# Kernel optimization log

Measured on AMD Instinct MI355X. Metric: run time of the kernel, lower is better.

The kernel has to match this reference:

```python
import jax, jax.numpy as jnp
import numpy as np

N_NODES = 100000
N_EDGES = 1600000
N_FEAT = 64
HIDDEN = 64
N_GRAPHS = 256


def setup_inputs() -> dict:
    key = jax.random.key(0)
    ks = jax.random.split(key, 8)
    x = jax.random.normal(ks[0], (N_NODES, N_FEAT), dtype=jnp.float32)
    edge_index = jax.random.randint(ks[1], (2, N_EDGES), 0, N_NODES, dtype=jnp.int64)
    batch = jnp.sort(jax.random.randint(ks[2], (N_NODES,), 0, N_GRAPHS, dtype=jnp.int64))
    W1 = jax.random.normal(ks[3], (N_FEAT, HIDDEN), dtype=jnp.float32) / np.sqrt(N_FEAT)
    b1 = jnp.zeros((HIDDEN,), dtype=jnp.float32)
    W2 = jax.random.normal(ks[4], (HIDDEN, HIDDEN), dtype=jnp.float32) / np.sqrt(HIDDEN)
    b2 = jnp.zeros((HIDDEN,), dtype=jnp.float32)
    Wfc = jax.random.normal(ks[5], (HIDDEN, 1), dtype=jnp.float32) / np.sqrt(HIDDEN)
    bfc = jnp.zeros((1,), dtype=jnp.float32)
    return {"x": x, "edge_index": edge_index, "batch": batch,
            "W1": W1, "b1": b1, "W2": W2, "b2": b2, "Wfc": Wfc, "bfc": bfc}


def _gcn_conv(x, W, b, src, dst, norm, n_nodes):
    # h = X W, then symmetric-normalized scatter-add aggregation at dst
    h = x @ W  # [N, H]
    msg = h[src] * norm[:, None]  # [E+N, H] gather + scale
    agg = jax.ops.segment_sum(msg, dst, num_segments=n_nodes)
    return agg + b


def reference(x, edge_index, batch, W1, b1, W2, b2, Wfc, bfc):
    n = x.shape[0]
    loops = jnp.arange(n, dtype=edge_index.dtype)
    src = jnp.concatenate([edge_index[0], loops])  # add self-loops (GCNConv default)
    dst = jnp.concatenate([edge_index[1], loops])
    deg = jax.ops.segment_sum(jnp.ones_like(dst, dtype=x.dtype), dst, num_segments=n)
    dinv = jnp.where(deg > 0, jax.lax.rsqrt(deg), 0.0)
    norm = dinv[src] * dinv[dst]  # D^-1/2 (A+I) D^-1/2

    h = jax.nn.relu(_gcn_conv(x, W1, b1, src, dst, norm, n))  # dropout = identity (eval)
    h = jax.nn.relu(_gcn_conv(h, W2, b2, src, dst, norm, n))

    # global mean pool over graphs
    sums = jax.ops.segment_sum(h, batch, num_segments=N_GRAPHS)
    counts = jax.ops.segment_sum(jnp.ones((n,), dtype=h.dtype), batch, num_segments=N_GRAPHS)
    pooled = sums / jnp.maximum(counts, 1.0)[:, None]  # [G, H]
    return jax.nn.sigmoid(pooled @ Wfc + bfc)  # [G, 1]
```

## Files before the change

kernel.cpp:

```cpp
#include <hip/hip_runtime.h>
#include <hip/hip_fp16.h>
#include <math.h>

#define N_NODES  100000
#define N_EDGES  1600000
#define NF       64
#define N_GRAPHS 256

#define BSH   7
#define NB    ((N_NODES + 127) / 128)
#define BCAP  2600

typedef float f32x2 __attribute__((ext_vector_type(2)));

__global__ void k_zerocur(int* __restrict__ bucketCur) {
    int i = blockIdx.x * blockDim.x + threadIdx.x;
    if (i < NB) bucketCur[i] = 0;
}

__global__ __launch_bounds__(1024) void k_bscatter(const int* __restrict__ src,
                                                   const int* __restrict__ dst,
                                                   int* __restrict__ bucketCur,
                                                   int* __restrict__ scratch) {
    __shared__ int hist[NB];
    __shared__ int bbase[NB];
    int t = threadIdx.x;
    for (int i = t; i < NB; i += 1024) hist[i] = 0;
    __syncthreads();
    int e0 = (blockIdx.x * 1024 + t) * 8;
    int d[8], s[8], r[8];
    bool act = (e0 + 7) < N_EDGES;
    if (act) {
        *(int4*)&d[0] = *(const int4*)(dst + e0);
        *(int4*)&d[4] = *(const int4*)(dst + e0 + 4);
        *(int4*)&s[0] = *(const int4*)(src + e0);
        *(int4*)&s[4] = *(const int4*)(src + e0 + 4);
#pragma unroll
        for (int k = 0; k < 8; ++k) r[k] = atomicAdd(&hist[d[k] >> BSH], 1);
    }
    __syncthreads();
    for (int i = t; i < NB; i += 1024)
        if (hist[i]) bbase[i] = atomicAdd(&bucketCur[i], hist[i]);
    __syncthreads();
    if (act) {
#pragma unroll
        for (int k = 0; k < 8; ++k) {
            int b = d[k] >> BSH;
            int pos = bbase[b] + r[k];
            if (pos < BCAP)
                scratch[b * BCAP + pos] = ((d[k] & 127) << 17) | s[k];
        }
    }
}

__global__ __launch_bounds__(1024) void k_bscan(const int* __restrict__ bucketCur,
                                                int* __restrict__ bucketPtr,
                                                int* __restrict__ rowptr) {
    int t = threadIdx.x;
    __shared__ int ps[1024];
    int v = (t < NB) ? min(bucketCur[t], BCAP) : 0;
    ps[t] = v;
    __syncthreads();
#pragma unroll
    for (int off = 1; off < 1024; off <<= 1) {
        int u = (t >= off) ? ps[t - off] : 0;
        __syncthreads();
        ps[t] += u;
        __syncthreads();
    }
    if (t < NB) bucketPtr[t] = ps[t] - v;
    if (t == NB - 1) {
        bucketPtr[NB] = ps[t];
        rowptr[N_NODES] = ps[t];
    }
}

__global__ __launch_bounds__(256) void k_bfinal(const int* __restrict__ bucketCur,
                                                const int* __restrict__ bucketPtr,
                                                const int* __restrict__ scratch,
                                                int* __restrict__ rowptr,
                                                float* __restrict__ dinv,
                                                int* __restrict__ col) {
    int b = blockIdx.x;
    int cnt  = min(bucketCur[b], BCAP);
    int base = bucketPtr[b];
    int node0 = b << BSH;
    __shared__ int hist[128];
    __shared__ int escan[128];
    __shared__ int ps[128];
    __shared__ int rnk[BCAP];
    int t = threadIdx.x;
    if (t < 128) hist[t] = 0;
    __syncthreads();
    const int* sp = scratch + b * BCAP;
    for (int j = t; j < cnt; j += 256)
        rnk[j] = atomicAdd(&hist[sp[j] >> 17], 1);
    __syncthreads();
    int hv = (t < 128) ? hist[t] : 0;
    if (t < 128) ps[t] = hv;
    __syncthreads();
#pragma unroll
    for (int off = 1; off < 128; off <<= 1) {
        int u = 0;
        if (t < 128 && t >= off) u = ps[t - off];
        __syncthreads();
        if (t < 128) ps[t] += u;
        __syncthreads();
    }
    if (t < 128) {
        int excl = ps[t] - hv;
        escan[t] = excl;
        int node = node0 + t;
        if (node < N_NODES) {
            rowptr[node] = base + excl;
            dinv[node] = rsqrtf((float)(hv + 1));
        }
    }
    __syncthreads();
    for (int j = t; j < cnt; j += 256) {
        int pk = sp[j];
        col[base + escan[pk >> 17] + rnk[j]] = pk & 0x1FFFF;
    }
}

__global__ __launch_bounds__(256) void k_gemm(const float* __restrict__ X,
                                              const float* __restrict__ W,
                                              const float* __restrict__ bias,
                                              const float* __restrict__ dinv,
                                              int* __restrict__ Ah8) {
    __shared__ float Ws[64][64];
    __shared__ float Xs[64][68];
    int t  = threadIdx.x;
    int n0 = blockIdx.x * 64;

    for (int i = t; i < 64 * 64; i += 256) Ws[i >> 6][i & 63] = W[i];

#pragma unroll
    for (int p = 0; p < 4; ++p) {
        int flat = p * 256 + t;
        int nl = flat >> 4;
        int kg = flat & 15;
        int node = n0 + nl;
        float4 v = make_float4(0.f, 0.f, 0.f, 0.f);
        if (node < N_NODES) {
            v = *(const float4*)(X + (size_t)node * NF + kg * 4);
            if (bias) {
                v.x += bias[kg * 4 + 0]; v.x = v.x > 0.f ? v.x : 0.f;
                v.y += bias[kg * 4 + 1]; v.y = v.y > 0.f ? v.y : 0.f;
                v.z += bias[kg * 4 + 2]; v.z = v.z > 0.f ? v.z : 0.f;
                v.w += bias[kg * 4 + 3]; v.w = v.w > 0.f ? v.w : 0.f;
            }
        }
        Xs[kg * 4 + 0][nl] = v.x;
        Xs[kg * 4 + 1][nl] = v.y;
        Xs[kg * 4 + 2][nl] = v.z;
        Xs[kg * 4 + 3][nl] = v.w;
    }
    __syncthreads();

    int tx = t & 15;
    int ty = t >> 4;
    float acc[4][4];
#pragma unroll
    for (int i = 0; i < 4; ++i)
#pragma unroll
        for (int j = 0; j < 4; ++j) acc[i][j] = 0.f;

#pragma unroll 8
    for (int k = 0; k < 64; ++k) {
        float4 wv = *(const float4*)&Ws[k][tx * 4];
        float4 xv = *(const float4*)&Xs[k][ty * 4];
        acc[0][0] += xv.x * wv.x; acc[0][1] += xv.x * wv.y;
        acc[0][2] += xv.x * wv.z; acc[0][3] += xv.x * wv.w;
        acc[1][0] += xv.y * wv.x; acc[1][1] += xv.y * wv.y;
        acc[1][2] += xv.y * wv.z; acc[1][3] += xv.y * wv.w;
        acc[2][0] += xv.z * wv.x; acc[2][1] += xv.z * wv.y;
        acc[2][2] += xv.z * wv.z; acc[2][3] += xv.z * wv.w;
        acc[3][0] += xv.w * wv.x; acc[3][1] += xv.w * wv.y;
        acc[3][2] += xv.w * wv.z; acc[3][3] += xv.w * wv.w;
    }

#pragma unroll
    for (int i = 0; i < 4; ++i) {
        int node = n0 + ty * 4 + i;
        if (node < N_NODES) {
            float dv = dinv[node];
            int pk = 0;
            pk = __builtin_amdgcn_cvt_pk_fp8_f32(acc[i][0] * dv, acc[i][1] * dv, pk, false);
            pk = __builtin_amdgcn_cvt_pk_fp8_f32(acc[i][2] * dv, acc[i][3] * dv, pk, true);
            Ah8[(size_t)node * 16 + tx] = pk;
        }
    }
}

__global__ __launch_bounds__(256) void k_pull(const int* __restrict__ rowptr,
                                              const int* __restrict__ col,
                                              const float* __restrict__ dinv,
                                              const int* __restrict__ Ah8,
                                              float* __restrict__ B) {
    int n    = (blockIdx.x * blockDim.x + threadIdx.x) >> 6;
    int lane = threadIdx.x & 63;
    if (n >= N_NODES) return;
    int slot = lane >> 3;
    int oct  = lane & 7;
    int beg = rowptr[n];
    int cnt = rowptr[n + 1] - beg + 1;

    float acc0 = 0.f, acc1 = 0.f, acc2 = 0.f, acc3 = 0.f;
    float acc4 = 0.f, acc5 = 0.f, acc6 = 0.f, acc7 = 0.f;

    for (int base = slot; base < cnt; base += 32) {
        int cidx[4];
#pragma unroll
        for (int p = 0; p < 4; ++p) {
            int idx = base + p * 8;
            cidx[p] = (idx < cnt) ? ((idx == 0) ? n : col[beg + idx - 1]) : -1;
        }
#pragma unroll
        for (int p = 0; p < 4; ++p) {
            int s = cidx[p];
            if (s >= 0) {
                int2 raw = *(const int2*)(Ah8 + (size_t)s * 16 + oct * 2);
                f32x2 f0 = __builtin_amdgcn_cvt_pk_f32_fp8(raw.x, false);
                f32x2 f1 = __builtin_amdgcn_cvt_pk_f32_fp8(raw.x, true);
                f32x2 f2 = __builtin_amdgcn_cvt_pk_f32_fp8(raw.y, false);
                f32x2 f3 = __builtin_amdgcn_cvt_pk_f32_fp8(raw.y, true);
                acc0 += f0.x; acc1 += f0.y;
                acc2 += f1.x; acc3 += f1.y;
                acc4 += f2.x; acc5 += f2.y;
                acc6 += f3.x; acc7 += f3.y;
            }
        }
    }
#pragma unroll
    for (int off = 8; off < 64; off <<= 1) {
        acc0 += __shfl_down(acc0, off);
        acc1 += __shfl_down(acc1, off);
        acc2 += __shfl_down(acc2, off);
        acc3 += __shfl_down(acc3, off);
        acc4 += __shfl_down(acc4, off);
        acc5 += __shfl_down(acc5, off);
        acc6 += __shfl_down(acc6, off);
        acc7 += __shfl_down(acc7, off);
    }
    if (slot == 0) {
        float dv = dinv[n];
        float4 o0 = make_float4(acc0 * dv, acc1 * dv, acc2 * dv, acc3 * dv);
        float4 o1 = make_float4(acc4 * dv, acc5 * dv, acc6 * dv, acc7 * dv);
        *(float4*)(B + (size_t)n * NF + oct * 8)     = o0;
        *(float4*)(B + (size_t)n * NF + oct * 8 + 4) = o1;
    }
}

__device__ __forceinline__ int lower_bound_i(const int* __restrict__ a, int n, int key) {
    int lo = 0, hi = n;
    while (lo < hi) {
        int mid = (lo + hi) >> 1;
        if (a[mid] < key) lo = mid + 1; else hi = mid;
    }
    return lo;
}

__global__ __launch_bounds__(512) void k_pool_final(const float* __restrict__ B,
                                                    const int* __restrict__ batch,
                                                    const float* __restrict__ b2,
                                                    const float* __restrict__ Wfc,
                                                    const float* __restrict__ bfc,
                                                    float* __restrict__ out) {
    int g = blockIdx.x;
    __shared__ int s_lo, s_hi;
    int t = threadIdx.x;
    if (t == 0) {
        s_lo = lower_bound_i(batch, N_NODES, g);
        s_hi = lower_bound_i(batch, N_NODES, g + 1);
    }
    __syncthreads();
    int lo = s_lo, hi = s_hi;
    int ln = t >> 6, lane = t & 63;
    float bias = b2[lane];
    float acc = 0.0f;
    for (int n = lo + ln; n < hi; n += 8) {
        float v = B[(size_t)n * NF + lane] + bias;
        acc += v > 0.0f ? v : 0.0f;
    }
    __shared__ float red[8][64];
    red[ln][lane] = acc;
    __syncthreads();
    if (ln == 0) {
        float tot = 0.0f;
#pragma unroll
        for (int w = 0; w < 8; ++w) tot += red[w][lane];
        int cnt = hi - lo;
        float c = cnt > 0 ? (float)cnt : 1.0f;
        float v = (tot / c) * Wfc[lane];
#pragma unroll
        for (int off = 32; off > 0; off >>= 1) v += __shfl_down(v, off);
        if (lane == 0) out[g] = 1.0f / (1.0f + expf(-(v + bfc[0])));
    }
}

extern "C" void kernel_launch(void* const* d_in, const int* in_sizes, int n_in,
                              void* d_out, int out_size, void* d_ws, size_t ws_size,
                              hipStream_t stream) {
    const float* x    = (const float*)d_in[0];
    const int*   ei   = (const int*)d_in[1];
    const int*   batch= (const int*)d_in[2];
    const float* W1   = (const float*)d_in[3];
    const float* b1   = (const float*)d_in[4];
    const float* W2   = (const float*)d_in[5];
    const float* b2   = (const float*)d_in[6];
    const float* Wfc  = (const float*)d_in[7];
    const float* bfc  = (const float*)d_in[8];
    float* out = (float*)d_out;

    const int* src = ei;
    const int* dst = ei + N_EDGES;

    float*  B         = (float*)d_ws;
    int*    Ah8       = (int*)(B + (size_t)N_NODES * NF);
    float*  dinv      = (float*)(Ah8 + (size_t)N_NODES * 16);
    int*    rowptr    = (int*)(dinv + N_NODES);
    int*    bucketCur = rowptr + N_NODES + 1;
    int*    bucketPtr = bucketCur + NB;
    int*    col       = bucketPtr + NB + 1;
    int*    scratch   = col + N_EDGES;

    const int BLK = 256;
    int g_gemm  = (N_NODES + 63) / 64;
    int g_nwave = (N_NODES + 3) / 4;
    int g_bsc   = (N_EDGES / 8 + 1023) / 1024;

    k_zerocur<<<(NB + BLK - 1) / BLK, BLK, 0, stream>>>(bucketCur);
    k_bscatter<<<g_bsc, 1024, 0, stream>>>(src, dst, bucketCur, scratch);
    k_bscan<<<1, 1024, 0, stream>>>(bucketCur, bucketPtr, rowptr);
    k_bfinal<<<NB, BLK, 0, stream>>>(bucketCur, bucketPtr, scratch, rowptr, dinv, col);

    k_gemm<<<g_gemm, BLK, 0, stream>>>(x, W1, nullptr, dinv, Ah8);
    k_pull<<<g_nwave, BLK, 0, stream>>>(rowptr, col, dinv, Ah8, B);

    k_gemm<<<g_gemm, BLK, 0, stream>>>(B, W2, b1, dinv, Ah8);
    k_pull<<<g_nwave, BLK, 0, stream>>>(rowptr, col, dinv, Ah8, B);

    k_pool_final<<<N_GRAPHS, 512, 0, stream>>>(B, batch, b2, Wfc, bfc, out);
}
```

Before: 259.4 us.

## Fuse aggregation with next GEMM and fold pooling plus FC projection into pull

Merges the first layer's neighbor aggregation with the second layer's GEMM, so the fp32 intermediate B is no longer written to and read back from global memory. The second aggregation now applies bias, ReLU and the Wfc dot product per node, then does a segmented reduction and atomically adds into per-graph sums. A tiny final kernel divides by graph counts and applies the sigmoid. The pull loops also change from 8 lanes per edge slot to one 8-lane group per node walking its edges sequentially, which shortens the reductions but may load-balance worse on high-degree nodes. Float atomics also make the summation order nondeterministic.

```diff
diff --git a/kernel.cpp b/kernel.cpp
--- a/kernel.cpp
+++ b/kernel.cpp
@@ -13,9 +13,10 @@
 
 typedef float f32x2 __attribute__((ext_vector_type(2)));
 
-__global__ void k_zerocur(int* __restrict__ bucketCur) {
+__global__ void k_zerocur(int* __restrict__ bucketCur, float* __restrict__ gsum) {
     int i = blockIdx.x * blockDim.x + threadIdx.x;
     if (i < NB) bucketCur[i] = 0;
+    if (i < N_GRAPHS) gsum[i] = 0.0f;
 }
 
 __global__ __launch_bounds__(1024) void k_bscatter(const int* __restrict__ src,
@@ -125,7 +126,6 @@
 
 __global__ __launch_bounds__(256) void k_gemm(const float* __restrict__ X,
                                               const float* __restrict__ W,
-                                              const float* __restrict__ bias,
                                               const float* __restrict__ dinv,
                                               int* __restrict__ Ah8) {
     __shared__ float Ws[64][64];
@@ -142,15 +142,8 @@
         int kg = flat & 15;
         int node = n0 + nl;
         float4 v = make_float4(0.f, 0.f, 0.f, 0.f);
-        if (node < N_NODES) {
+        if (node < N_NODES)
             v = *(const float4*)(X + (size_t)node * NF + kg * 4);
-            if (bias) {
-                v.x += bias[kg * 4 + 0]; v.x = v.x > 0.f ? v.x : 0.f;
-                v.y += bias[kg * 4 + 1]; v.y = v.y > 0.f ? v.y : 0.f;
-                v.z += bias[kg * 4 + 2]; v.z = v.z > 0.f ? v.z : 0.f;
-                v.w += bias[kg * 4 + 3]; v.w = v.w > 0.f ? v.w : 0.f;
-            }
-        }
         Xs[kg * 4 + 0][nl] = v.x;
         Xs[kg * 4 + 1][nl] = v.y;
         Xs[kg * 4 + 2][nl] = v.z;
@@ -193,63 +186,224 @@
     }
 }
 
-__global__ __launch_bounds__(256) void k_pull(const int* __restrict__ rowptr,
-                                              const int* __restrict__ col,
-                                              const float* __restrict__ dinv,
-                                              const int* __restrict__ Ah8,
-                                              float* __restrict__ B) {
-    int n    = (blockIdx.x * blockDim.x + threadIdx.x) >> 6;
-    int lane = threadIdx.x & 63;
-    if (n >= N_NODES) return;
-    int slot = lane >> 3;
-    int oct  = lane & 7;
-    int beg = rowptr[n];
-    int cnt = rowptr[n + 1] - beg + 1;
-
-    float acc0 = 0.f, acc1 = 0.f, acc2 = 0.f, acc3 = 0.f;
-    float acc4 = 0.f, acc5 = 0.f, acc6 = 0.f, acc7 = 0.f;
-
-    for (int base = slot; base < cnt; base += 32) {
-        int cidx[4];
-#pragma unroll
-        for (int p = 0; p < 4; ++p) {
-            int idx = base + p * 8;
-            cidx[p] = (idx < cnt) ? ((idx == 0) ? n : col[beg + idx - 1]) : -1;
-        }
-#pragma unroll
-        for (int p = 0; p < 4; ++p) {
-            int s = cidx[p];
-            if (s >= 0) {
-                int2 raw = *(const int2*)(Ah8 + (size_t)s * 16 + oct * 2);
-                f32x2 f0 = __builtin_amdgcn_cvt_pk_f32_fp8(raw.x, false);
-                f32x2 f1 = __builtin_amdgcn_cvt_pk_f32_fp8(raw.x, true);
-                f32x2 f2 = __builtin_amdgcn_cvt_pk_f32_fp8(raw.y, false);
-                f32x2 f3 = __builtin_amdgcn_cvt_pk_f32_fp8(raw.y, true);
-                acc0 += f0.x; acc1 += f0.y;
-                acc2 += f1.x; acc3 += f1.y;
-                acc4 += f2.x; acc5 += f2.y;
-                acc6 += f3.x; acc7 += f3.y;
+__global__ __launch_bounds__(256) void k_pullgemm(const int* __restrict__ rowptr,
+                                                  const int* __restrict__ col,
+                                                  const float* __restrict__ dinv,
+                                                  const int* __restrict__ Ah8,
+                                                  const float* __restrict__ W,
+                                                  const float* __restrict__ bias,
+                                                  int* __restrict__ AhOut) {
+    __shared__ float Ws[64][64];
+    __shared__ float Xs[64][68];
+    int t  = threadIdx.x;
+    int n0 = blockIdx.x * 64;
+
+    for (int i = t; i < 64 * 64; i += 256) Ws[i >> 6][i & 63] = W[i];
+
+    int wv      = t >> 6;
+    int lane    = t & 63;
+    int nodeSub = lane >> 3;
+    int oct     = lane & 7;
+
+    float4 bA = *(const float4*)(bias + oct * 8);
+    float4 bB = *(const float4*)(bias + oct * 8 + 4);
+
+#pragma unroll
+    for (int r = 0; r < 2; ++r) {
+        int nl = wv * 16 + r * 8 + nodeSub;
+        int n  = n0 + nl;
+        f32x2 a0 = {0.f, 0.f}, a1 = {0.f, 0.f}, a2 = {0.f, 0.f}, a3 = {0.f, 0.f};
+        float dv = 0.f;
+        if (n < N_NODES) {
+            int beg = rowptr[n];
+            int cnt = rowptr[n + 1] - beg;
+            dv = dinv[n];
+            {
+                int2 raw = *(const int2*)(Ah8 + (size_t)n * 16 + oct * 2);
+                a0 += __builtin_amdgcn_cvt_pk_f32_fp8(raw.x, false);
+                a1 += __builtin_amdgcn_cvt_pk_f32_fp8(raw.x, true);
+                a2 += __builtin_amdgcn_cvt_pk_f32_fp8(raw.y, false);
+                a3 += __builtin_amdgcn_cvt_pk_f32_fp8(raw.y, true);
             }
-        }
-    }
+            int e = 0;
+            for (; e + 4 <= cnt; e += 4) {
+                int c0 = col[beg + e + 0];
+                int c1 = col[beg + e + 1];
+                int c2 = col[beg + e + 2];
+                int c3 = col[beg + e + 3];
+                int2 r0 = *(const int2*)(Ah8 + (size_t)c0 * 16 + oct * 2);
+                int2 r1 = *(const int2*)(Ah8 + (size_t)c1 * 16 + oct * 2);
+                int2 r2 = *(const int2*)(Ah8 + (size_t)c2 * 16 + oct * 2);
+                int2 r3 = *(const int2*)(Ah8 + (size_t)c3 * 16 + oct * 2);
+                a0 += __builtin_amdgcn_cvt_pk_f32_fp8(r0.x, false);
+                a1 += __builtin_amdgcn_cvt_pk_f32_fp8(r0.x, true);
+                a2 += __builtin_amdgcn_cvt_pk_f32_fp8(r0.y, false);
+                a3 += __builtin_amdgcn_cvt_pk_f32_fp8(r0.y, true);
+                a0 += __builtin_amdgcn_cvt_pk_f32_fp8(r1.x, false);
+                a1 += __builtin_amdgcn_cvt_pk_f32_fp8(r1.x, true);
+                a2 += __builtin_amdgcn_cvt_pk_f32_fp8(r1.y, false);
+                a3 += __builtin_amdgcn_cvt_pk_f32_fp8(r1.y, true);
+                a0 += __builtin_amdgcn_cvt_pk_f32_fp8(r2.x, false);
+                a1 += __builtin_amdgcn_cvt_pk_f32_fp8(r2.x, true);
+                a2 += __builtin_amdgcn_cvt_pk_f32_fp8(r2.y, false);
+                a3 += __builtin_amdgcn_cvt_pk_f32_fp8(r2.y, true);
+                a0 += __builtin_amdgcn_cvt_pk_f32_fp8(r3.x, false);
+                a1 += __builtin_amdgcn_cvt_pk_f32_fp8(r3.x, true);
+                a2 += __builtin_amdgcn_cvt_pk_f32_fp8(r3.y, false);
+                a3 += __builtin_amdgcn_cvt_pk_f32_fp8(r3.y, true);
+            }
+            for (; e < cnt; ++e) {
+                int c0 = col[beg + e];
+                int2 r0 = *(const int2*)(Ah8 + (size_t)c0 * 16 + oct * 2);
+                a0 += __builtin_amdgcn_cvt_pk_f32_fp8(r0.x, false);
+                a1 += __builtin_amdgcn_cvt_pk_f32_fp8(r0.x, true);
+                a2 += __builtin_amdgcn_cvt_pk_f32_fp8(r0.y, false);
+                a3 += __builtin_amdgcn_cvt_pk_f32_fp8(r0.y, true);
+            }
+        }
+        float f0 = a0.x * dv + bA.x; Xs[oct * 8 + 0][nl] = f0 > 0.f ? f0 : 0.f;
+        float f1 = a0.y * dv + bA.y; Xs[oct * 8 + 1][nl] = f1 > 0.f ? f1 : 0.f;
+        float f2 = a1.x * dv + bA.z; Xs[oct * 8 + 2][nl] = f2 > 0.f ? f2 : 0.f;
+        float f3 = a1.y * dv + bA.w; Xs[oct * 8 + 3][nl] = f3 > 0.f ? f3 : 0.f;
+        float f4 = a2.x * dv + bB.x; Xs[oct * 8 + 4][nl] = f4 > 0.f ? f4 : 0.f;
+        float f5 = a2.y * dv + bB.y; Xs[oct * 8 + 5][nl] = f5 > 0.f ? f5 : 0.f;
+        float f6 = a3.x * dv + bB.z; Xs[oct * 8 + 6][nl] = f6 > 0.f ? f6 : 0.f;
+        float f7 = a3.y * dv + bB.w; Xs[oct * 8 + 7][nl] = f7 > 0.f ? f7 : 0.f;
+    }
+    __syncthreads();
+
+    int tx = t & 15;
+    int ty = t >> 4;
+    float acc[4][4];
+#pragma unroll
+    for (int i = 0; i < 4; ++i)
+#pragma unroll
+        for (int j = 0; j < 4; ++j) acc[i][j] = 0.f;
+
+#pragma unroll 8
+    for (int k = 0; k < 64; ++k) {
+        float4 wvv = *(const float4*)&Ws[k][tx * 4];
+        float4 xv  = *(const float4*)&Xs[k][ty * 4];
+        acc[0][0] += xv.x * wvv.x; acc[0][1] += xv.x * wvv.y;
+        acc[0][2] += xv.x * wvv.z; acc[0][3] += xv.x * wvv.w;
+        acc[1][0] += xv.y * wvv.x; acc[1][1] += xv.y * wvv.y;
+        acc[1][2] += xv.y * wvv.z; acc[1][3] += xv.y * wvv.w;
+        acc[2][0] += xv.z * wvv.x; acc[2][1] += xv.z * wvv.y;
+        acc[2][2] += xv.z * wvv.z; acc[2][3] += xv.z * wvv.w;
+        acc[3][0] += xv.w * wvv.x; acc[3][1] += xv.w * wvv.y;
+        acc[3][2] += xv.w * wvv.z; acc[3][3] += xv.w * wvv.w;
+    }
+
+#pragma unroll
+    for (int i = 0; i < 4; ++i) {
+        int node = n0 + ty * 4 + i;
+        if (node < N_NODES) {
+            float dv = dinv[node];
+            int pk = 0;
+            pk = __builtin_amdgcn_cvt_pk_fp8_f32(acc[i][0] * dv, acc[i][1] * dv, pk, false);
+            pk = __builtin_amdgcn_cvt_pk_fp8_f32(acc[i][2] * dv, acc[i][3] * dv, pk, true);
+            AhOut[(size_t)node * 16 + tx] = pk;
+        }
+    }
+}
+
+__global__ __launch_bounds__(256) void k_pullpool(const int* __restrict__ rowptr,
+                                                  const int* __restrict__ col,
+                                                  const float* __restrict__ dinv,
+                                                  const int* __restrict__ Ah8,
+                                                  const float* __restrict__ b2,
+                                                  const float* __restrict__ Wfc,
+                                                  const int* __restrict__ batch,
+                                                  float* __restrict__ gsum) {
+    int t       = threadIdx.x;
+    int lane    = t & 63;
+    int wv      = t >> 6;
+    int nodeSub = lane >> 3;
+    int oct     = lane & 7;
+    int n = blockIdx.x * 32 + wv * 8 + nodeSub;
+
+    float4 bA = *(const float4*)(b2 + oct * 8);
+    float4 bB = *(const float4*)(b2 + oct * 8 + 4);
+    float4 wA = *(const float4*)(Wfc + oct * 8);
+    float4 wB = *(const float4*)(Wfc + oct * 8 + 4);
+
+    float s = 0.f;
+    int   g = -1;
+    if (n < N_NODES) {
+        g = batch[n];
+        int beg = rowptr[n];
+        int cnt = rowptr[n + 1] - beg;
+        f32x2 a0 = {0.f, 0.f}, a1 = {0.f, 0.f}, a2 = {0.f, 0.f}, a3 = {0.f, 0.f};
+        {
+            int2 raw = *(const int2*)(Ah8 + (size_t)n * 16 + oct * 2);
+            a0 += __builtin_amdgcn_cvt_pk_f32_fp8(raw.x, false);
+            a1 += __builtin_amdgcn_cvt_pk_f32_fp8(raw.x, true);
+            a2 += __builtin_amdgcn_cvt_pk_f32_fp8(raw.y, false);
+            a3 += __builtin_amdgcn_cvt_pk_f32_fp8(raw.y, true);
+        }
+        int e = 0;
+        for (; e + 4 <= cnt; e += 4) {
+            int c0 = col[beg + e + 0];
+            int c1 = col[beg + e + 1];
+            int c2 = col[beg + e + 2];
+            int c3 = col[beg + e + 3];
+            int2 r0 = *(const int2*)(Ah8 + (size_t)c0 * 16 + oct * 2);
+            int2 r1 = *(const int2*)(Ah8 + (size_t)c1 * 16 + oct * 2);
+            int2 r2 = *(const int2*)(Ah8 + (size_t)c2 * 16 + oct * 2);
+            int2 r3 = *(const int2*)(Ah8 + (size_t)c3 * 16 + oct * 2);
+            a0 += __builtin_amdgcn_cvt_pk_f32_fp8(r0.x, false);
+            a1 += __builtin_amdgcn_cvt_pk_f32_fp8(r0.x, true);
+            a2 += __builtin_amdgcn_cvt_pk_f32_fp8(r0.y, false);
+            a3 += __builtin_amdgcn_cvt_pk_f32_fp8(r0.y, true);
+            a0 += __builtin_amdgcn_cvt_pk_f32_fp8(r1.x, false);
+            a1 += __builtin_amdgcn_cvt_pk_f32_fp8(r1.x, true);
+            a2 += __builtin_amdgcn_cvt_pk_f32_fp8(r1.y, false);
+            a3 += __builtin_amdgcn_cvt_pk_f32_fp8(r1.y, true);
+            a0 += __builtin_amdgcn_cvt_pk_f32_fp8(r2.x, false);
+            a1 += __builtin_amdgcn_cvt_pk_f32_fp8(r2.x, true);
+            a2 += __builtin_amdgcn_cvt_pk_f32_fp8(r2.y, false);
+            a3 += __builtin_amdgcn_cvt_pk_f32_fp8(r2.y, true);
+            a0 += __builtin_amdgcn_cvt_pk_f32_fp8(r3.x, false);
+            a1 += __builtin_amdgcn_cvt_pk_f32_fp8(r3.x, true);
+            a2 += __builtin_amdgcn_cvt_pk_f32_fp8(r3.y, false);
+            a3 += __builtin_amdgcn_cvt_pk_f32_fp8(r3.y, true);
+        }
+        for (; e < cnt; ++e) {
+            int c0 = col[beg + e];
+            int2 r0 = *(const int2*)(Ah8 + (size_t)c0 * 16 + oct * 2);
+            a0 += __builtin_amdgcn_cvt_pk_f32_fp8(r0.x, false);
+            a1 += __builtin_amdgcn_cvt_pk_f32_fp8(r0.x, true);
+            a2 += __builtin_amdgcn_cvt_pk_f32_fp8(r0.y, false);
+            a3 += __builtin_amdgcn_cvt_pk_f32_fp8(r0.y, true);
+        }
+        float dv = dinv[n];
+        float wsum = 0.f;
+        float v;
+        v = a0.x * dv + bA.x; wsum += (v > 0.f ? v : 0.f) * wA.x;
+        v = a0.y * dv + bA.y; wsum += (v > 0.f ? v : 0.f) * wA.y;
+        v = a1.x * dv + bA.z; wsum += (v > 0.f ? v : 0.f) * wA.z;
+        v = a1.y * dv + bA.w; wsum += (v > 0.f ? v : 0.f) * wA.w;
+        v = a2.x * dv + bB.x; wsum += (v > 0.f ? v : 0.f) * wB.x;
+        v = a2.y * dv + bB.y; wsum += (v > 0.f ? v : 0.f) * wB.y;
+        v = a3.x * dv + bB.z; wsum += (v > 0.f ? v : 0.f) * wB.z;
+        v = a3.y * dv + bB.w; wsum += (v > 0.f ? v : 0.f) * wB.w;
+        wsum += __shfl_xor(wsum, 1);
+        wsum += __shfl_xor(wsum, 2);
+        wsum += __shfl_xor(wsum, 4);
+        s = wsum;
+    }
+
+    float sv = (oct == 0) ? s : 0.f;
+    int   gv = (oct == 0) ? g : -2;
 #pragma unroll
     for (int off = 8; off < 64; off <<= 1) {
-        acc0 += __shfl_down(acc0, off);
-        acc1 += __shfl_down(acc1, off);
-        acc2 += __shfl_down(acc2, off);
-        acc3 += __shfl_down(acc3, off);
-        acc4 += __shfl_down(acc4, off);
-        acc5 += __shfl_down(acc5, off);
-        acc6 += __shfl_down(acc6, off);
-        acc7 += __shfl_down(acc7, off);
-    }
-    if (slot == 0) {
-        float dv = dinv[n];
-        float4 o0 = make_float4(acc0 * dv, acc1 * dv, acc2 * dv, acc3 * dv);
-        float4 o1 = make_float4(acc4 * dv, acc5 * dv, acc6 * dv, acc7 * dv);
-        *(float4*)(B + (size_t)n * NF + oct * 8)     = o0;
-        *(float4*)(B + (size_t)n * NF + oct * 8 + 4) = o1;
-    }
+        float s2 = __shfl_down(sv, off);
+        int   g2 = __shfl_down(gv, off);
+        if (g2 == gv) sv += s2;
+    }
+    int gp = __shfl_up(gv, 8);
+    bool head = (lane < 8) || (gp != gv);
+    if (oct == 0 && g >= 0 && head) atomicAdd(&gsum[g], sv);
 }
 
 __device__ __forceinline__ int lower_bound_i(const int* __restrict__ a, int n, int key) {
@@ -261,41 +415,17 @@
     return lo;
 }
 
-__global__ __launch_bounds__(512) void k_pool_final(const float* __restrict__ B,
-                                                    const int* __restrict__ batch,
-                                                    const float* __restrict__ b2,
-                                                    const float* __restrict__ Wfc,
-                                                    const float* __restrict__ bfc,
-                                                    float* __restrict__ out) {
-    int g = blockIdx.x;
-    __shared__ int s_lo, s_hi;
-    int t = threadIdx.x;
-    if (t == 0) {
-        s_lo = lower_bound_i(batch, N_NODES, g);
-        s_hi = lower_bound_i(batch, N_NODES, g + 1);
-    }
-    __syncthreads();
-    int lo = s_lo, hi = s_hi;
-    int ln = t >> 6, lane = t & 63;
-    float bias = b2[lane];
-    float acc = 0.0f;
-    for (int n = lo + ln; n < hi; n += 8) {
-        float v = B[(size_t)n * NF + lane] + bias;
-        acc += v > 0.0f ? v : 0.0f;
-    }
-    __shared__ float red[8][64];
-    red[ln][lane] = acc;
-    __syncthreads();
-    if (ln == 0) {
-        float tot = 0.0f;
-#pragma unroll
-        for (int w = 0; w < 8; ++w) tot += red[w][lane];
-        int cnt = hi - lo;
-        float c = cnt > 0 ? (float)cnt : 1.0f;
-        float v = (tot / c) * Wfc[lane];
-#pragma unroll
-        for (int off = 32; off > 0; off >>= 1) v += __shfl_down(v, off);
-        if (lane == 0) out[g] = 1.0f / (1.0f + expf(-(v + bfc[0])));
+__global__ void k_final(const int* __restrict__ batch,
+                        const float* __restrict__ gsum,
+                        const float* __restrict__ bfc,
+                        float* __restrict__ out) {
+    int g = blockIdx.x * blockDim.x + threadIdx.x;
+    if (g < N_GRAPHS) {
+        int lo = lower_bound_i(batch, N_NODES, g);
+        int hi = lower_bound_i(batch, N_NODES, g + 1);
+        float c = (hi > lo) ? (float)(hi - lo) : 1.0f;
+        float v = gsum[g] / c + bfc[0];
+        out[g] = 1.0f / (1.0f + expf(-v));
     }
 }
 
@@ -316,30 +446,30 @@
     const int* src = ei;
     const int* dst = ei + N_EDGES;
 
-    float*  B         = (float*)d_ws;
-    int*    Ah8       = (int*)(B + (size_t)N_NODES * NF);
-    float*  dinv      = (float*)(Ah8 + (size_t)N_NODES * 16);
+    int*    Ah8       = (int*)d_ws;
+    int*    Ah8b      = Ah8 + (size_t)N_NODES * 16;
+    float*  dinv      = (float*)(Ah8b + (size_t)N_NODES * 16);
     int*    rowptr    = (int*)(dinv + N_NODES);
     int*    bucketCur = rowptr + N_NODES + 1;
     int*    bucketPtr = bucketCur + NB;
     int*    col       = bucketPtr + NB + 1;
-    int*    scratch   = col + N_EDGES;
+    float*  gsum      = (float*)(col + N_EDGES);
+    int*    scratch   = (int*)(gsum + N_GRAPHS);
 
     const int BLK = 256;
-    int g_gemm  = (N_NODES + 63) / 64;
-    int g_nwave = (N_NODES + 3) / 4;
-    int g_bsc   = (N_EDGES / 8 + 1023) / 1024;
-
-    k_zerocur<<<(NB + BLK - 1) / BLK, BLK, 0, stream>>>(bucketCur);
+    int g_gemm = (N_NODES + 63) / 64;
+    int g_pp   = (N_NODES + 31) / 32;
+    int g_bsc  = (N_EDGES / 8 + 1023) / 1024;
+
+    k_zerocur<<<(NB + BLK - 1) / BLK, BLK, 0, stream>>>(bucketCur, gsum);
     k_bscatter<<<g_bsc, 1024, 0, stream>>>(src, dst, bucketCur, scratch);
     k_bscan<<<1, 1024, 0, stream>>>(bucketCur, bucketPtr, rowptr);
     k_bfinal<<<NB, BLK, 0, stream>>>(bucketCur, bucketPtr, scratch, rowptr, dinv, col);
 
-    k_gemm<<<g_gemm, BLK, 0, stream>>>(x, W1, nullptr, dinv, Ah8);
-    k_pull<<<g_nwave, BLK, 0, stream>>>(rowptr, col, dinv, Ah8, B);
-
-    k_gemm<<<g_gemm, BLK, 0, stream>>>(B, W2, b1, dinv, Ah8);
-    k_pull<<<g_nwave, BLK, 0, stream>>>(rowptr, col, dinv, Ah8, B);
-
-    k_pool_final<<<N_GRAPHS, 512, 0, stream>>>(B, batch, b2, Wfc, bfc, out);
-}
+    k_gemm<<<g_gemm, BLK, 0, stream>>>(x, W1, dinv, Ah8);
+
+    k_pullgemm<<<g_gemm, BLK, 0, stream>>>(rowptr, col, dinv, Ah8, W2, b1, Ah8b);
+
+    k_pullpool<<<g_pp, BLK, 0, stream>>>(rowptr, col, dinv, Ah8b, b2, Wfc, batch, gsum);
+    k_final<<<1, BLK, 0, stream>>>(batch, gsum, bfc, out);
+}
```

Result: faster. 238.0 us (-8.3%).
